# Optimization experiments

Measured on AMD Instinct MI355X. Metric: run time of the kernel, lower is better.

Reference implementation:

```python
import jax, jax.numpy as jnp
import numpy as np

NEG_INF = -1e30


def setup_inputs() -> dict:
    key = jax.random.key(0)
    kq, kk, kv, ks = jax.random.split(key, 4)
    B, H, S, D = 2, 16, 2048, 64
    return {
        "q": jax.random.normal(kq, (B, H, S, D), dtype=jnp.float32),
        "k": jax.random.normal(kk, (B, H, S, D), dtype=jnp.float32),
        "v": jax.random.normal(kv, (B, H, S, D), dtype=jnp.float32),
        "sink_weights": jax.random.normal(ks, (H,), dtype=jnp.float32),
        "sliding_window": 1024,
    }


def reference(q, k, v, sink_weights, sliding_window):
    """Sliding-window causal attention with a learnable attention-sink logit.

    Equivalent to FlexAttention.forward with sink_weights given: an extra kv
    position (the sink) is appended whose score is replaced by sink_weights[h]
    and whose value is zero -> it only adds mass to the softmax denominator.
    """
    B, H, S_q, D = q.shape
    S_kv = k.shape[2]
    scale = 1.0 / np.sqrt(D)

    # [B, H, S_q, S_kv] raw scores
    scores = jnp.einsum("bhqd,bhkd->bhqk", q, k) * scale

    q_idx = jnp.arange(S_q)[:, None]
    kv_idx = jnp.arange(S_kv)[None, :]
    keep = (kv_idx <= q_idx) & (q_idx - kv_idx <= sliding_window)  # [S_q, S_kv]
    scores = jnp.where(keep[None, None], scores, NEG_INF)

    # sink column: per-head learnable logit, always visible
    sink_col = jnp.broadcast_to(
        sink_weights[None, :, None, None], (B, H, S_q, 1)
    )
    logits = jnp.concatenate([scores, sink_col], axis=-1)  # [B,H,S_q,S_kv+1]

    probs = jax.nn.softmax(logits, axis=-1)
    # sink value is zero, so only the first S_kv prob columns hit v
    out = jnp.einsum("bhqk,bhkd->bhqd", probs[..., :S_kv], v)
    return out
```

## Files before the change

### kernel.cpp

```cpp
#include <hip/hip_runtime.h>


typedef __bf16 bf16x8 __attribute__((ext_vector_type(8)));
typedef __bf16 bf16x4 __attribute__((ext_vector_type(4)));
typedef float  f32x16 __attribute__((ext_vector_type(16)));

#define NT 256
#define NEG_BIG (-3.0e38f)

__device__ __forceinline__ int swz(int row, int gran) {
    return row * 64 + ((gran ^ ((row >> 1) & 7)) << 3);
}

__device__ __forceinline__ bf16x4 xswap32(bf16x4 v) {
    union { bf16x4 v; int i[2]; } u;
    u.v = v;
    u.i[0] = __shfl_xor(u.i[0], 32, 64);
    u.i[1] = __shfl_xor(u.i[1], 32, 64);
    return u.v;
}

__device__ const int SEG_N[24] = {3,2,2,2,2,1,2,1, 1,1,1,1,1,1,1,1, 1,1,1,1,1,1,1,1};
__device__ const int SEG_IT[24][3] = {
  {0,1,2},{2,3,0},{3,4,0},{4,5,0},{5,6,0},{6,0,0},{6,7,0},{7,0,0},
  {8,0,0},{8,0,0},{9,0,0},{9,0,0},{10,0,0},{10,0,0},{11,0,0},{11,0,0},
  {12,0,0},{12,0,0},{13,0,0},{13,0,0},{14,0,0},{14,0,0},{15,0,0},{15,0,0}};
__device__ const int SEG_J0[24][3] = {
  {0,0,0},{3,0,0},{6,0,0},{7,0,0},{6,0,0},{3,0,0},{12,0,0},{7,0,0},
  {0,0,0},{9,0,0},{0,0,0},{9,0,0},{0,0,0},{9,0,0},{0,0,0},{9,0,0},
  {0,0,0},{9,0,0},{0,0,0},{9,0,0},{0,0,0},{9,0,0},{0,0,0},{9,0,0}};
__device__ const int SEG_J1[24][3] = {
  {2,4,3},{6,6,0},{8,7,0},{10,6,0},{12,3,0},{12,0,0},{14,7,0},{16,0,0},
  {9,0,0},{18,0,0},{9,0,0},{18,0,0},{9,0,0},{18,0,0},{9,0,0},{18,0,0},
  {9,0,0},{18,0,0},{9,0,0},{18,0,0},{9,0,0},{18,0,0},{9,0,0},{18,0,0}};
__device__ const int SEG_SX[24][3] = {
  {0,0,0},{1,0,0},{1,0,0},{1,0,0},{1,0,0},{1,0,0},{2,0,0},{1,0,0},
  {0,0,0},{1,0,0},{0,0,0},{1,0,0},{0,0,0},{1,0,0},{0,0,0},{1,0,0},
  {0,0,0},{1,0,0},{0,0,0},{1,0,0},{0,0,0},{1,0,0},{0,0,0},{1,0,0}};
__device__ const int NSEG_ITEM[16] = {1,1,2,2,2,2,3,2, 2,2,2,2,2,2,2,2};

__global__ __launch_bounds__(NT, 3) void flex_r13_main(
    const float* __restrict__ Q, const float* __restrict__ K,
    const float* __restrict__ V, const float* __restrict__ SINKW,
    const int* __restrict__ SWIN, void* __restrict__ WS,
    float* __restrict__ OUT, const int H, const int S)
{
    const int t    = threadIdx.x;
    const int lane = t & 63;
    const int w    = t >> 6;
    const int c    = lane & 31;
    const int hl   = lane >> 5;
    const int W    = SWIN[0];
    const float scale = 0.125f;

    const int NBH = gridDim.x / 24;
    int bh, b24;
    if ((NBH & 7) == 0) {
        const int xcd  = blockIdx.x & 7;
        const int rest = blockIdx.x >> 3;
        const int G    = NBH >> 3;
        bh  = (rest % G) * 8 + xcd;
        b24 = rest / G;
    } else {
        bh  = blockIdx.x / 24;
        b24 = blockIdx.x - bh * 24;
    }
    const int h   = bh % H;
    const float sw = SINKW[h];

    __shared__ __align__(16) __bf16 k_lds[2][64 * 64];
    __shared__ __align__(16) __bf16 v_lds[2][64 * 64];

    const size_t basebh = (size_t)bh * S * 64;
    const float4* kp4 = (const float4*)(K + basebh);
    const float4* vp4 = (const float4*)(V + basebh);
    __bf16* O_ws  = (__bf16*)WS;
    float2* ml_ws = (float2*)((char*)WS + (size_t)NBH * 48 * 16384);

    const int dgi = t & 15;
    const int kgi = t >> 4;
    float4 kreg[4], vreg[4];

    const int ns = SEG_N[b24];

    {
        const int it0 = SEG_IT[b24][0];
        const int ktA0 = (2 * it0 - 16 > 0) ? (2 * it0 - 16) : 0;
        const int kt = ktA0 + SEG_J0[b24][0];
        #pragma unroll
        for (int i = 0; i < 4; ++i) kreg[i] = kp4[kt * 1024 + i * NT + t];
        #pragma unroll
        for (int kk = 0; kk < 4; ++kk) vreg[kk] = vp4[kt * 1024 + (4 * kgi + kk) * 16 + dgi];
        #pragma unroll
        for (int i = 0; i < 4; ++i) {
            const int flat = i * NT + t;
            const int key = flat >> 4, dd = flat & 15;
            float4 f = kreg[i];
            bf16x4 b = { (__bf16)f.x, (__bf16)f.y, (__bf16)f.z, (__bf16)f.w };
            *(bf16x4*)&k_lds[0][swz(key, dd >> 1) + (dd & 1) * 4] = b;
        }
        {
            float4 a0 = vreg[0], a1 = vreg[1], a2 = vreg[2], a3 = vreg[3];
            bf16x4 w0 = { (__bf16)a0.x, (__bf16)a1.x, (__bf16)a2.x, (__bf16)a3.x };
            bf16x4 w1 = { (__bf16)a0.y, (__bf16)a1.y, (__bf16)a2.y, (__bf16)a3.y };
            bf16x4 w2 = { (__bf16)a0.z, (__bf16)a1.z, (__bf16)a2.z, (__bf16)a3.z };
            bf16x4 w3 = { (__bf16)a0.w, (__bf16)a1.w, (__bf16)a2.w, (__bf16)a3.w };
            const int gv = kgi >> 1, ov = (kgi & 1) * 4;
            *(bf16x4*)&v_lds[0][swz(4 * dgi + 0, gv) + ov] = w0;
            *(bf16x4*)&v_lds[0][swz(4 * dgi + 1, gv) + ov] = w1;
            *(bf16x4*)&v_lds[0][swz(4 * dgi + 2, gv) + ov] = w2;
            *(bf16x4*)&v_lds[0][swz(4 * dgi + 3, gv) + ov] = w3;
        }
    }

    int par = 0;

    for (int s = 0; s < ns; ++s) {
        const int item = SEG_IT[b24][s];
        const int j0   = SEG_J0[b24][s];
        const int j1   = SEG_J1[b24][s];
        const int sidx = SEG_SX[b24][s];
        const int ktA  = (2 * item - 16 > 0) ? (2 * item - 16) : 0;
        const int qw0  = item * 128 + 32 * w;
        const int qi   = qw0 + c;

        bf16x8 bq[4];
        {
            const float4* qp4 = (const float4*)(Q + basebh + (size_t)qi * 64);
            #pragma unroll
            for (int ks = 0; ks < 4; ++ks) {
                float4 f0 = qp4[4 * ks + 2 * hl];
                float4 f1 = qp4[4 * ks + 2 * hl + 1];
                bq[ks][0] = (__bf16)(f0.x * scale); bq[ks][1] = (__bf16)(f0.y * scale);
                bq[ks][2] = (__bf16)(f0.z * scale); bq[ks][3] = (__bf16)(f0.w * scale);
                bq[ks][4] = (__bf16)(f1.x * scale); bq[ks][5] = (__bf16)(f1.y * scale);
                bq[ks][6] = (__bf16)(f1.z * scale); bq[ks][7] = (__bf16)(f1.w * scale);
            }
        }

        float mrun = (sidx == 0) ? sw : NEG_BIG;
        float lrun = (sidx == 0) ? 1.0f : 0.0f;
        f32x16 accO0, accO1;
        #pragma unroll
        for (int i = 0; i < 16; ++i) { accO0[i] = 0.0f; accO1[i] = 0.0f; }

        for (int j = j0; j < j1; ++j) {
            const int k0 = (ktA + j) * 64;

            __syncthreads();

            int nkt = -1;
            if (j + 1 < j1) nkt = ktA + j + 1;
            else if (s + 1 < ns) {
                const int it2 = SEG_IT[b24][s + 1];
                const int ktA2 = (2 * it2 - 16 > 0) ? (2 * it2 - 16) : 0;
                nkt = ktA2 + SEG_J0[b24][s + 1];
            }
            if (nkt >= 0) {
                #pragma unroll
                for (int i = 0; i < 4; ++i) kreg[i] = kp4[nkt * 1024 + i * NT + t];
                #pragma unroll
                for (int kk = 0; kk < 4; ++kk) vreg[kk] = vp4[nkt * 1024 + (4 * kgi + kk) * 16 + dgi];
            }

            const __bf16* kb = k_lds[par];
            const __bf16* vb = v_lds[par];
            f32x16 accS0, accS1;
            #pragma unroll
            for (int i = 0; i < 16; ++i) { accS0[i] = 0.0f; accS1[i] = 0.0f; }
            __builtin_amdgcn_s_setprio(1);
            #pragma unroll
            for (int ks = 0; ks < 4; ++ks) {
                bf16x8 ka0 = *(const bf16x8*)&kb[swz(c,      2 * ks + hl)];
                bf16x8 ka1 = *(const bf16x8*)&kb[swz(32 + c, 2 * ks + hl)];
                accS0 = __builtin_amdgcn_mfma_f32_32x32x16_bf16(ka0, bq[ks], accS0, 0, 0, 0);
                accS1 = __builtin_amdgcn_mfma_f32_32x32x16_bf16(ka1, bq[ks], accS1, 0, 0, 0);
            }
            __builtin_amdgcn_s_setprio(0);

            const bool interior = (k0 + 63 <= qw0) && (qw0 + 31 - k0 <= W);
            if (!interior) {
                #pragma unroll
                for (int rg = 0; rg < 16; ++rg) {
                    const int kb2 = (rg & 3) + 8 * (rg >> 2) + 4 * hl;
                    const int ki0 = k0 + kb2, ki1 = k0 + 32 + kb2;
                    if (!((ki0 <= qi) && (qi - ki0 <= W))) accS0[rg] = -1e30f;
                    if (!((ki1 <= qi) && (qi - ki1 <= W))) accS1[rg] = -1e30f;
                }
            }

            float q4[8];
            #pragma unroll
            for (int i = 0; i < 4; ++i) {
                q4[i]   = fmaxf(fmaxf(accS0[4*i], accS0[4*i+1]),
                                fmaxf(accS0[4*i+2], accS0[4*i+3]));
                q4[4+i] = fmaxf(fmaxf(accS1[4*i], accS1[4*i+1]),
                                fmaxf(accS1[4*i+2], accS1[4*i+3]));
            }
            float mx = fmaxf(fmaxf(fmaxf(q4[0], q4[1]), fmaxf(q4[2], q4[3])),
                             fmaxf(fmaxf(q4[4], q4[5]), fmaxf(q4[6], q4[7])));
            mx = fmaxf(mx, __shfl_xor(mx, 32, 64));
            if (!__all(mx <= mrun + 8.0f)) {
                const float mnew  = fmaxf(mrun, mx);
                const float alpha = __expf(mrun - mnew);
                lrun *= alpha;
                #pragma unroll
                for (int i = 0; i < 16; ++i) { accO0[i] *= alpha; accO1[i] *= alpha; }
                mrun = mnew;
            }
            float ps = 0.0f;
            #pragma unroll
            for (int i = 0; i < 16; ++i) { float p = __expf(accS0[i] - mrun); accS0[i] = p; ps += p; }
            #pragma unroll
            for (int i = 0; i < 16; ++i) { float p = __expf(accS1[i] - mrun); accS1[i] = p; ps += p; }
            ps += __shfl_xor(ps, 32, 64);
            lrun += ps;

            bf16x4 qA = { (__bf16)accS0[0],  (__bf16)accS0[1],  (__bf16)accS0[2],  (__bf16)accS0[3]  };
            bf16x4 qB = { (__bf16)accS0[4],  (__bf16)accS0[5],  (__bf16)accS0[6],  (__bf16)accS0[7]  };
            bf16x4 qC = { (__bf16)accS0[8],  (__bf16)accS0[9],  (__bf16)accS0[10], (__bf16)accS0[11] };
            bf16x4 qD = { (__bf16)accS0[12], (__bf16)accS0[13], (__bf16)accS0[14], (__bf16)accS0[15] };
            bf16x4 qE = { (__bf16)accS1[0],  (__bf16)accS1[1],  (__bf16)accS1[2],  (__bf16)accS1[3]  };
            bf16x4 qF = { (__bf16)accS1[4],  (__bf16)accS1[5],  (__bf16)accS1[6],  (__bf16)accS1[7]  };
            bf16x4 qG = { (__bf16)accS1[8],  (__bf16)accS1[9],  (__bf16)accS1[10], (__bf16)accS1[11] };
            bf16x4 qH = { (__bf16)accS1[12], (__bf16)accS1[13], (__bf16)accS1[14], (__bf16)accS1[15] };
            bf16x4 r0 = xswap32(hl ? qA : qB);
            bf16x4 r1 = xswap32(hl ? qC : qD);
            bf16x4 r2 = xswap32(hl ? qE : qF);
            bf16x4 r3 = xswap32(hl ? qG : qH);
            bf16x4 lo0 = hl ? r0 : qA, hi0 = hl ? qB : r0;
            bf16x4 lo1 = hl ? r1 : qC, hi1 = hl ? qD : r1;
            bf16x4 lo2 = hl ? r2 : qE, hi2 = hl ? qF : r2;
            bf16x4 lo3 = hl ? r3 : qG, hi3 = hl ? qH : r3;
            bf16x8 bp[4];
            #pragma unroll
            for (int e = 0; e < 4; ++e) {
                bp[0][e] = lo0[e]; bp[0][4+e] = hi0[e];
                bp[1][e] = lo1[e]; bp[1][4+e] = hi1[e];
                bp[2][e] = lo2[e]; bp[2][4+e] = hi2[e];
                bp[3][e] = lo3[e]; bp[3][4+e] = hi3[e];
            }

            __builtin_amdgcn_s_setprio(1);
            #pragma unroll
            for (int ks = 0; ks < 4; ++ks) {
                bf16x8 va0 = *(const bf16x8*)&vb[swz(c,      2 * ks + hl)];
                bf16x8 va1 = *(const bf16x8*)&vb[swz(32 + c, 2 * ks + hl)];
                accO0 = __builtin_amdgcn_mfma_f32_32x32x16_bf16(va0, bp[ks], accO0, 0, 0, 0);
                accO1 = __builtin_amdgcn_mfma_f32_32x32x16_bf16(va1, bp[ks], accO1, 0, 0, 0);
            }
            __builtin_amdgcn_s_setprio(0);

            if (nkt >= 0) {
                const int np = par ^ 1;
                #pragma unroll
                for (int i = 0; i < 4; ++i) {
                    const int flat = i * NT + t;
                    const int key = flat >> 4, dd = flat & 15;
                    float4 f = kreg[i];
                    bf16x4 b = { (__bf16)f.x, (__bf16)f.y, (__bf16)f.z, (__bf16)f.w };
                    *(bf16x4*)&k_lds[np][swz(key, dd >> 1) + (dd & 1) * 4] = b;
                }
                float4 a0 = vreg[0], a1 = vreg[1], a2 = vreg[2], a3 = vreg[3];
                bf16x4 w0 = { (__bf16)a0.x, (__bf16)a1.x, (__bf16)a2.x, (__bf16)a3.x };
                bf16x4 w1 = { (__bf16)a0.y, (__bf16)a1.y, (__bf16)a2.y, (__bf16)a3.y };
                bf16x4 w2 = { (__bf16)a0.z, (__bf16)a1.z, (__bf16)a2.z, (__bf16)a3.z };
                bf16x4 w3 = { (__bf16)a0.w, (__bf16)a1.w, (__bf16)a2.w, (__bf16)a3.w };
                const int gv = kgi >> 1, ov = (kgi & 1) * 4;
                *(bf16x4*)&v_lds[np][swz(4 * dgi + 0, gv) + ov] = w0;
                *(bf16x4*)&v_lds[np][swz(4 * dgi + 1, gv) + ov] = w1;
                *(bf16x4*)&v_lds[np][swz(4 * dgi + 2, gv) + ov] = w2;
                *(bf16x4*)&v_lds[np][swz(4 * dgi + 3, gv) + ov] = w3;
            }
            par ^= 1;
        }

        if (item < 2) {
            const float inv = 1.0f / lrun;
            float* ob = OUT + basebh + (size_t)qi * 64;
            #pragma unroll
            for (int rg = 0; rg < 4; ++rg) {
                float4 f0 = { accO0[4*rg+0]*inv, accO0[4*rg+1]*inv,
                              accO0[4*rg+2]*inv, accO0[4*rg+3]*inv };
                float4 f1 = { accO1[4*rg+0]*inv, accO1[4*rg+1]*inv,
                              accO1[4*rg+2]*inv, accO1[4*rg+3]*inv };
                *(float4*)&ob[     8 * rg + 4 * hl] = f0;
                *(float4*)&ob[32 + 8 * rg + 4 * hl] = f1;
            }
        } else {
            const int slot = (bh * 16 + item) * 3 + sidx;
            const int qrel = 32 * w + c;
            if (hl == 0) ml_ws[(size_t)slot * 128 + qrel] = make_float2(mrun, lrun);
            __bf16* Os = O_ws + (size_t)slot * 8192 + (size_t)qrel * 64;
            #pragma unroll
            for (int qd = 0; qd < 4; ++qd) {
                const int d0 = 8 * qd + 4 * hl;
                bf16x4 b0 = { (__bf16)accO0[4*qd+0], (__bf16)accO0[4*qd+1],
                              (__bf16)accO0[4*qd+2], (__bf16)accO0[4*qd+3] };
                bf16x4 b1 = { (__bf16)accO1[4*qd+0], (__bf16)accO1[4*qd+1],
                              (__bf16)accO1[4*qd+2], (__bf16)accO1[4*qd+3] };
                *(bf16x4*)&Os[d0]      = b0;
                *(bf16x4*)&Os[32 + d0] = b1;
            }
        }
    }
}

__global__ __launch_bounds__(256) void flex_r13_combine(
    const void* __restrict__ WS, float* __restrict__ OUT, const int H, const int S)
{
    const int NBH  = gridDim.x / 14;
    const int bi   = blockIdx.x;
    const int bh   = bi / 14;
    const int item = 2 + (bi - bh * 14);
    const int ns   = NSEG_ITEM[item];
    const int t    = threadIdx.x;
    const int q    = t >> 1;
    const int half = t & 1;

    const __bf16* O_ws = (const __bf16*)WS;
    const float2* ml_ws = (const float2*)((const char*)WS + (size_t)NBH * 48 * 16384);
    const int base = (bh * 16 + item) * 3;

    float m[3], lv[3], a[3];
    float mst = NEG_BIG;
    for (int s = 0; s < ns; ++s) {
        float2 e = ml_ws[(size_t)(base + s) * 128 + q];
        m[s] = e.x; lv[s] = e.y;
        mst = fmaxf(mst, m[s]);
    }
    float lst = 0.0f;
    for (int s = 0; s < ns; ++s) { a[s] = __expf(m[s] - mst); lst += a[s] * lv[s]; }
    const float inv = 1.0f / lst;

    float acc[32];
    #pragma unroll
    for (int i = 0; i < 32; ++i) acc[i] = 0.0f;
    for (int s = 0; s < ns; ++s) {
        const __bf16* Os = O_ws + (size_t)(base + s) * 8192 + (size_t)q * 64 + 32 * half;
        const float as = a[s];
        #pragma unroll
        for (int v8 = 0; v8 < 4; ++v8) {
            bf16x8 o = *(const bf16x8*)&Os[8 * v8];
            #pragma unroll
            for (int jj = 0; jj < 8; ++jj) acc[8 * v8 + jj] += as * (float)o[jj];
        }
    }

    float* dst = OUT + (size_t)bh * S * 64 + (size_t)(item * 128 + q) * 64 + 32 * half;
    #pragma unroll
    for (int v4 = 0; v4 < 8; ++v4) {
        float4 f = { acc[4*v4+0] * inv, acc[4*v4+1] * inv,
                     acc[4*v4+2] * inv, acc[4*v4+3] * inv };
        *(float4*)&dst[4 * v4] = f;
    }
}

extern "C" void kernel_launch(void* const* d_in, const int* in_sizes, int n_in,
                              void* d_out, int out_size, void* d_ws, size_t ws_size,
                              hipStream_t stream) {
    const float* q     = (const float*)d_in[0];
    const float* k     = (const float*)d_in[1];
    const float* v     = (const float*)d_in[2];
    const float* sinkw = (const float*)d_in[3];
    const int*   swin  = (const int*)d_in[4];
    float* out = (float*)d_out;

    const int H = in_sizes[3];
    const int S = 2048;
    const int B = in_sizes[0] / (H * S * 64);
    const int NBH = B * H;

    flex_r13_main<<<dim3(NBH * 24), NT, 0, stream>>>(q, k, v, sinkw, swin, d_ws, out, H, S);
    flex_r13_combine<<<dim3(NBH * 14), 256, 0, stream>>>(d_ws, out, H, S);
}
```

Before: 131.2 us.

## Process two KV tiles per iteration with one shared softmax max and rescale

The inner loop now handles two 64-key tiles per step. Both tiles are staged in a double-buffered LDS layout, and one running max and rescale is computed across the pair, which halves the barriers and max-update checks per key. Exp sums are split into several partial accumulators to shorten dependency chains. The cost is double the LDS and register footprint, and launch bounds drop from 3 to 2 blocks per SM, which reduces occupancy.

```diff
diff --git a/kernel.cpp b/kernel.cpp
--- a/kernel.cpp
+++ b/kernel.cpp
@@ -39,7 +39,91 @@
   {0,0,0},{1,0,0},{0,0,0},{1,0,0},{0,0,0},{1,0,0},{0,0,0},{1,0,0}};
 __device__ const int NSEG_ITEM[16] = {1,1,2,2,2,2,3,2, 2,2,2,2,2,2,2,2};
 
-__global__ __launch_bounds__(NT, 3) void flex_r13_main(
+__device__ __forceinline__ void qk_mfma(const __bf16* kb, const bf16x8 bq[4],
+                                        int c, int hl, f32x16& s0, f32x16& s1) {
+    #pragma unroll
+    for (int ks = 0; ks < 4; ++ks) {
+        bf16x8 ka0 = *(const bf16x8*)&kb[swz(c,      2 * ks + hl)];
+        bf16x8 ka1 = *(const bf16x8*)&kb[swz(32 + c, 2 * ks + hl)];
+        s0 = __builtin_amdgcn_mfma_f32_32x32x16_bf16(ka0, bq[ks], s0, 0, 0, 0);
+        s1 = __builtin_amdgcn_mfma_f32_32x32x16_bf16(ka1, bq[ks], s1, 0, 0, 0);
+    }
+}
+
+__device__ __forceinline__ void pv_mfma(const __bf16* vb, const bf16x8 bp[4],
+                                        int c, int hl, f32x16& o0, f32x16& o1) {
+    #pragma unroll
+    for (int ks = 0; ks < 4; ++ks) {
+        bf16x8 va0 = *(const bf16x8*)&vb[swz(c,      2 * ks + hl)];
+        bf16x8 va1 = *(const bf16x8*)&vb[swz(32 + c, 2 * ks + hl)];
+        o0 = __builtin_amdgcn_mfma_f32_32x32x16_bf16(va0, bp[ks], o0, 0, 0, 0);
+        o1 = __builtin_amdgcn_mfma_f32_32x32x16_bf16(va1, bp[ks], o1, 0, 0, 0);
+    }
+}
+
+__device__ __forceinline__ void mask_tile(f32x16& s0, f32x16& s1,
+                                          int k0, int qi, int W, int hl) {
+    #pragma unroll
+    for (int rg = 0; rg < 16; ++rg) {
+        const int kb2 = (rg & 3) + 8 * (rg >> 2) + 4 * hl;
+        const int ki0 = k0 + kb2, ki1 = k0 + 32 + kb2;
+        if (!((ki0 <= qi) && (qi - ki0 <= W))) s0[rg] = -1e30f;
+        if (!((ki1 <= qi) && (qi - ki1 <= W))) s1[rg] = -1e30f;
+    }
+}
+
+__device__ __forceinline__ void exch_bp(const f32x16 s0, const f32x16 s1,
+                                        int hl, bf16x8 bp[4]) {
+    bf16x4 qA = { (__bf16)s0[0],  (__bf16)s0[1],  (__bf16)s0[2],  (__bf16)s0[3]  };
+    bf16x4 qB = { (__bf16)s0[4],  (__bf16)s0[5],  (__bf16)s0[6],  (__bf16)s0[7]  };
+    bf16x4 qC = { (__bf16)s0[8],  (__bf16)s0[9],  (__bf16)s0[10], (__bf16)s0[11] };
+    bf16x4 qD = { (__bf16)s0[12], (__bf16)s0[13], (__bf16)s0[14], (__bf16)s0[15] };
+    bf16x4 qE = { (__bf16)s1[0],  (__bf16)s1[1],  (__bf16)s1[2],  (__bf16)s1[3]  };
+    bf16x4 qF = { (__bf16)s1[4],  (__bf16)s1[5],  (__bf16)s1[6],  (__bf16)s1[7]  };
+    bf16x4 qG = { (__bf16)s1[8],  (__bf16)s1[9],  (__bf16)s1[10], (__bf16)s1[11] };
+    bf16x4 qH = { (__bf16)s1[12], (__bf16)s1[13], (__bf16)s1[14], (__bf16)s1[15] };
+    bf16x4 r0 = xswap32(hl ? qA : qB);
+    bf16x4 r1 = xswap32(hl ? qC : qD);
+    bf16x4 r2 = xswap32(hl ? qE : qF);
+    bf16x4 r3 = xswap32(hl ? qG : qH);
+    bf16x4 lo0 = hl ? r0 : qA, hi0 = hl ? qB : r0;
+    bf16x4 lo1 = hl ? r1 : qC, hi1 = hl ? qD : r1;
+    bf16x4 lo2 = hl ? r2 : qE, hi2 = hl ? qF : r2;
+    bf16x4 lo3 = hl ? r3 : qG, hi3 = hl ? qH : r3;
+    #pragma unroll
+    for (int e = 0; e < 4; ++e) {
+        bp[0][e] = lo0[e]; bp[0][4+e] = hi0[e];
+        bp[1][e] = lo1[e]; bp[1][4+e] = hi1[e];
+        bp[2][e] = lo2[e]; bp[2][4+e] = hi2[e];
+        bp[3][e] = lo3[e]; bp[3][4+e] = hi3[e];
+    }
+}
+
+__device__ __forceinline__ void stage_k(__bf16* dst, const float4* kr, int t) {
+    #pragma unroll
+    for (int i = 0; i < 4; ++i) {
+        const int flat = i * NT + t;
+        const int key = flat >> 4, dd = flat & 15;
+        float4 f = kr[i];
+        bf16x4 b = { (__bf16)f.x, (__bf16)f.y, (__bf16)f.z, (__bf16)f.w };
+        *(bf16x4*)&dst[swz(key, dd >> 1) + (dd & 1) * 4] = b;
+    }
+}
+
+__device__ __forceinline__ void stage_v(__bf16* dst, const float4* vr, int dgi, int kgi) {
+    float4 a0 = vr[0], a1 = vr[1], a2 = vr[2], a3 = vr[3];
+    bf16x4 w0 = { (__bf16)a0.x, (__bf16)a1.x, (__bf16)a2.x, (__bf16)a3.x };
+    bf16x4 w1 = { (__bf16)a0.y, (__bf16)a1.y, (__bf16)a2.y, (__bf16)a3.y };
+    bf16x4 w2 = { (__bf16)a0.z, (__bf16)a1.z, (__bf16)a2.z, (__bf16)a3.z };
+    bf16x4 w3 = { (__bf16)a0.w, (__bf16)a1.w, (__bf16)a2.w, (__bf16)a3.w };
+    const int gv = kgi >> 1, ov = (kgi & 1) * 4;
+    *(bf16x4*)&dst[swz(4 * dgi + 0, gv) + ov] = w0;
+    *(bf16x4*)&dst[swz(4 * dgi + 1, gv) + ov] = w1;
+    *(bf16x4*)&dst[swz(4 * dgi + 2, gv) + ov] = w2;
+    *(bf16x4*)&dst[swz(4 * dgi + 3, gv) + ov] = w3;
+}
+
+__global__ __launch_bounds__(NT, 2) void flex_r14_main(
     const float* __restrict__ Q, const float* __restrict__ K,
     const float* __restrict__ V, const float* __restrict__ SINKW,
     const int* __restrict__ SWIN, void* __restrict__ WS,
@@ -68,8 +152,8 @@
     const int h   = bh % H;
     const float sw = SINKW[h];
 
-    __shared__ __align__(16) __bf16 k_lds[2][64 * 64];
-    __shared__ __align__(16) __bf16 v_lds[2][64 * 64];
+    __shared__ __align__(16) __bf16 k_lds[2][2][64 * 64];
+    __shared__ __align__(16) __bf16 v_lds[2][2][64 * 64];
 
     const size_t basebh = (size_t)bh * S * 64;
     const float4* kp4 = (const float4*)(K + basebh);
@@ -79,38 +163,28 @@
 
     const int dgi = t & 15;
     const int kgi = t >> 4;
-    float4 kreg[4], vreg[4];
+    float4 kreg[8], vreg[8];
 
     const int ns = SEG_N[b24];
 
     {
         const int it0 = SEG_IT[b24][0];
         const int ktA0 = (2 * it0 - 16 > 0) ? (2 * it0 - 16) : 0;
-        const int kt = ktA0 + SEG_J0[b24][0];
-        #pragma unroll
-        for (int i = 0; i < 4; ++i) kreg[i] = kp4[kt * 1024 + i * NT + t];
-        #pragma unroll
-        for (int kk = 0; kk < 4; ++kk) vreg[kk] = vp4[kt * 1024 + (4 * kgi + kk) * 16 + dgi];
+        const int kt0 = ktA0 + SEG_J0[b24][0];
         #pragma unroll
         for (int i = 0; i < 4; ++i) {
-            const int flat = i * NT + t;
-            const int key = flat >> 4, dd = flat & 15;
-            float4 f = kreg[i];
-            bf16x4 b = { (__bf16)f.x, (__bf16)f.y, (__bf16)f.z, (__bf16)f.w };
-            *(bf16x4*)&k_lds[0][swz(key, dd >> 1) + (dd & 1) * 4] = b;
-        }
-        {
-            float4 a0 = vreg[0], a1 = vreg[1], a2 = vreg[2], a3 = vreg[3];
-            bf16x4 w0 = { (__bf16)a0.x, (__bf16)a1.x, (__bf16)a2.x, (__bf16)a3.x };
-            bf16x4 w1 = { (__bf16)a0.y, (__bf16)a1.y, (__bf16)a2.y, (__bf16)a3.y };
-            bf16x4 w2 = { (__bf16)a0.z, (__bf16)a1.z, (__bf16)a2.z, (__bf16)a3.z };
-            bf16x4 w3 = { (__bf16)a0.w, (__bf16)a1.w, (__bf16)a2.w, (__bf16)a3.w };
-            const int gv = kgi >> 1, ov = (kgi & 1) * 4;
-            *(bf16x4*)&v_lds[0][swz(4 * dgi + 0, gv) + ov] = w0;
-            *(bf16x4*)&v_lds[0][swz(4 * dgi + 1, gv) + ov] = w1;
-            *(bf16x4*)&v_lds[0][swz(4 * dgi + 2, gv) + ov] = w2;
-            *(bf16x4*)&v_lds[0][swz(4 * dgi + 3, gv) + ov] = w3;
-        }
+            kreg[i]     = kp4[kt0 * 1024 + i * NT + t];
+            kreg[4 + i] = kp4[(kt0 + 1) * 1024 + i * NT + t];
+        }
+        #pragma unroll
+        for (int kk = 0; kk < 4; ++kk) {
+            vreg[kk]     = vp4[kt0 * 1024 + (4 * kgi + kk) * 16 + dgi];
+            vreg[4 + kk] = vp4[(kt0 + 1) * 1024 + (4 * kgi + kk) * 16 + dgi];
+        }
+        stage_k(&k_lds[0][0][0], &kreg[0], t);
+        stage_v(&v_lds[0][0][0], &vreg[0], dgi, kgi);
+        stage_k(&k_lds[0][1][0], &kreg[4], t);
+        stage_v(&v_lds[0][1][0], &vreg[4], dgi, kgi);
     }
 
     int par = 0;
@@ -144,61 +218,68 @@
         #pragma unroll
         for (int i = 0; i < 16; ++i) { accO0[i] = 0.0f; accO1[i] = 0.0f; }
 
-        for (int j = j0; j < j1; ++j) {
-            const int k0 = (ktA + j) * 64;
+        for (int j = j0; j < j1; j += 2) {
+            const bool two = (j + 1 < j1);
+            const int k0a = (ktA + j) * 64;
+            const int k0b = k0a + 64;
 
             __syncthreads();
 
-            int nkt = -1;
-            if (j + 1 < j1) nkt = ktA + j + 1;
-            else if (s + 1 < ns) {
-                const int it2 = SEG_IT[b24][s + 1];
+            int n0 = -1, n1 = -1;
+            if (j + 2 < j1) {
+                n0 = ktA + j + 2;
+                if (j + 3 < j1) n1 = n0 + 1;
+            } else if (s + 1 < ns) {
+                const int it2  = SEG_IT[b24][s + 1];
                 const int ktA2 = (2 * it2 - 16 > 0) ? (2 * it2 - 16) : 0;
-                nkt = ktA2 + SEG_J0[b24][s + 1];
-            }
-            if (nkt >= 0) {
-                #pragma unroll
-                for (int i = 0; i < 4; ++i) kreg[i] = kp4[nkt * 1024 + i * NT + t];
-                #pragma unroll
-                for (int kk = 0; kk < 4; ++kk) vreg[kk] = vp4[nkt * 1024 + (4 * kgi + kk) * 16 + dgi];
-            }
-
-            const __bf16* kb = k_lds[par];
-            const __bf16* vb = v_lds[par];
-            f32x16 accS0, accS1;
-            #pragma unroll
-            for (int i = 0; i < 16; ++i) { accS0[i] = 0.0f; accS1[i] = 0.0f; }
+                const int j02  = SEG_J0[b24][s + 1];
+                n0 = ktA2 + j02;
+                if (j02 + 1 < SEG_J1[b24][s + 1]) n1 = n0 + 1;
+            }
+            if (n0 >= 0) {
+                #pragma unroll
+                for (int i = 0; i < 4; ++i) kreg[i] = kp4[n0 * 1024 + i * NT + t];
+                #pragma unroll
+                for (int kk = 0; kk < 4; ++kk) vreg[kk] = vp4[n0 * 1024 + (4 * kgi + kk) * 16 + dgi];
+            }
+            if (n1 >= 0) {
+                #pragma unroll
+                for (int i = 0; i < 4; ++i) kreg[4 + i] = kp4[n1 * 1024 + i * NT + t];
+                #pragma unroll
+                for (int kk = 0; kk < 4; ++kk) vreg[4 + kk] = vp4[n1 * 1024 + (4 * kgi + kk) * 16 + dgi];
+            }
+
+            f32x16 sa0, sa1, sb0, sb1;
+            #pragma unroll
+            for (int i = 0; i < 16; ++i) { sa0[i] = 0.0f; sa1[i] = 0.0f; sb0[i] = 0.0f; sb1[i] = 0.0f; }
             __builtin_amdgcn_s_setprio(1);
-            #pragma unroll
-            for (int ks = 0; ks < 4; ++ks) {
-                bf16x8 ka0 = *(const bf16x8*)&kb[swz(c,      2 * ks + hl)];
-                bf16x8 ka1 = *(const bf16x8*)&kb[swz(32 + c, 2 * ks + hl)];
-                accS0 = __builtin_amdgcn_mfma_f32_32x32x16_bf16(ka0, bq[ks], accS0, 0, 0, 0);
-                accS1 = __builtin_amdgcn_mfma_f32_32x32x16_bf16(ka1, bq[ks], accS1, 0, 0, 0);
-            }
+            qk_mfma(&k_lds[par][0][0], bq, c, hl, sa0, sa1);
+            if (two) qk_mfma(&k_lds[par][1][0], bq, c, hl, sb0, sb1);
             __builtin_amdgcn_s_setprio(0);
 
-            const bool interior = (k0 + 63 <= qw0) && (qw0 + 31 - k0 <= W);
-            if (!interior) {
-                #pragma unroll
-                for (int rg = 0; rg < 16; ++rg) {
-                    const int kb2 = (rg & 3) + 8 * (rg >> 2) + 4 * hl;
-                    const int ki0 = k0 + kb2, ki1 = k0 + 32 + kb2;
-                    if (!((ki0 <= qi) && (qi - ki0 <= W))) accS0[rg] = -1e30f;
-                    if (!((ki1 <= qi) && (qi - ki1 <= W))) accS1[rg] = -1e30f;
+            if (!((k0a + 63 <= qw0) && (qw0 + 31 - k0a <= W)))
+                mask_tile(sa0, sa1, k0a, qi, W, hl);
+            if (two && !((k0b + 63 <= qw0) && (qw0 + 31 - k0b <= W)))
+                mask_tile(sb0, sb1, k0b, qi, W, hl);
+
+            float m8[8];
+            #pragma unroll
+            for (int i = 0; i < 4; ++i) {
+                m8[i]   = fmaxf(fmaxf(sa0[4*i], sa0[4*i+1]), fmaxf(sa0[4*i+2], sa0[4*i+3]));
+                m8[4+i] = fmaxf(fmaxf(sa1[4*i], sa1[4*i+1]), fmaxf(sa1[4*i+2], sa1[4*i+3]));
+            }
+            float mx = fmaxf(fmaxf(fmaxf(m8[0], m8[1]), fmaxf(m8[2], m8[3])),
+                             fmaxf(fmaxf(m8[4], m8[5]), fmaxf(m8[6], m8[7])));
+            if (two) {
+                float n8[8];
+                #pragma unroll
+                for (int i = 0; i < 4; ++i) {
+                    n8[i]   = fmaxf(fmaxf(sb0[4*i], sb0[4*i+1]), fmaxf(sb0[4*i+2], sb0[4*i+3]));
+                    n8[4+i] = fmaxf(fmaxf(sb1[4*i], sb1[4*i+1]), fmaxf(sb1[4*i+2], sb1[4*i+3]));
                 }
-            }
-
-            float q4[8];
-            #pragma unroll
-            for (int i = 0; i < 4; ++i) {
-                q4[i]   = fmaxf(fmaxf(accS0[4*i], accS0[4*i+1]),
-                                fmaxf(accS0[4*i+2], accS0[4*i+3]));
-                q4[4+i] = fmaxf(fmaxf(accS1[4*i], accS1[4*i+1]),
-                                fmaxf(accS1[4*i+2], accS1[4*i+3]));
-            }
-            float mx = fmaxf(fmaxf(fmaxf(q4[0], q4[1]), fmaxf(q4[2], q4[3])),
-                             fmaxf(fmaxf(q4[4], q4[5]), fmaxf(q4[6], q4[7])));
+                mx = fmaxf(mx, fmaxf(fmaxf(fmaxf(n8[0], n8[1]), fmaxf(n8[2], n8[3])),
+                                     fmaxf(fmaxf(n8[4], n8[5]), fmaxf(n8[6], n8[7]))));
+            }
             mx = fmaxf(mx, __shfl_xor(mx, 32, 64));
             if (!__all(mx <= mrun + 8.0f)) {
                 const float mnew  = fmaxf(mrun, mx);
@@ -208,69 +289,47 @@
                 for (int i = 0; i < 16; ++i) { accO0[i] *= alpha; accO1[i] *= alpha; }
                 mrun = mnew;
             }
-            float ps = 0.0f;
-            #pragma unroll
-            for (int i = 0; i < 16; ++i) { float p = __expf(accS0[i] - mrun); accS0[i] = p; ps += p; }
-            #pragma unroll
-            for (int i = 0; i < 16; ++i) { float p = __expf(accS1[i] - mrun); accS1[i] = p; ps += p; }
+            float sc[8];
+            #pragma unroll
+            for (int i = 0; i < 8; ++i) sc[i] = 0.0f;
+            #pragma unroll
+            for (int i = 0; i < 16; ++i) {
+                float p0 = __expf(sa0[i] - mrun); sa0[i] = p0; sc[i & 3]       += p0;
+                float p1 = __expf(sa1[i] - mrun); sa1[i] = p1; sc[4 + (i & 3)] += p1;
+            }
+            if (two) {
+                #pragma unroll
+                for (int i = 0; i < 16; ++i) {
+                    float p0 = __expf(sb0[i] - mrun); sb0[i] = p0; sc[i & 3]       += p0;
+                    float p1 = __expf(sb1[i] - mrun); sb1[i] = p1; sc[4 + (i & 3)] += p1;
+                }
+            }
+            float ps = ((sc[0] + sc[1]) + (sc[2] + sc[3])) + ((sc[4] + sc[5]) + (sc[6] + sc[7]));
             ps += __shfl_xor(ps, 32, 64);
             lrun += ps;
 
-            bf16x4 qA = { (__bf16)accS0[0],  (__bf16)accS0[1],  (__bf16)accS0[2],  (__bf16)accS0[3]  };
-            bf16x4 qB = { (__bf16)accS0[4],  (__bf16)accS0[5],  (__bf16)accS0[6],  (__bf16)accS0[7]  };
-            bf16x4 qC = { (__bf16)accS0[8],  (__bf16)accS0[9],  (__bf16)accS0[10], (__bf16)accS0[11] };
-            bf16x4 qD = { (__bf16)accS0[12], (__bf16)accS0[13], (__bf16)accS0[14], (__bf16)accS0[15] };
-            bf16x4 qE = { (__bf16)accS1[0],  (__bf16)accS1[1],  (__bf16)accS1[2],  (__bf16)accS1[3]  };
-            bf16x4 qF = { (__bf16)accS1[4],  (__bf16)accS1[5],  (__bf16)accS1[6],  (__bf16)accS1[7]  };
-            bf16x4 qG = { (__bf16)accS1[8],  (__bf16)accS1[9],  (__bf16)accS1[10], (__bf16)accS1[11] };
-            bf16x4 qH = { (__bf16)accS1[12], (__bf16)accS1[13], (__bf16)accS1[14], (__bf16)accS1[15] };
-            bf16x4 r0 = xswap32(hl ? qA : qB);
-            bf16x4 r1 = xswap32(hl ? qC : qD);
-            bf16x4 r2 = xswap32(hl ? qE : qF);
-            bf16x4 r3 = xswap32(hl ? qG : qH);
-            bf16x4 lo0 = hl ? r0 : qA, hi0 = hl ? qB : r0;
-            bf16x4 lo1 = hl ? r1 : qC, hi1 = hl ? qD : r1;
-            bf16x4 lo2 = hl ? r2 : qE, hi2 = hl ? qF : r2;
-            bf16x4 lo3 = hl ? r3 : qG, hi3 = hl ? qH : r3;
-            bf16x8 bp[4];
-            #pragma unroll
-            for (int e = 0; e < 4; ++e) {
-                bp[0][e] = lo0[e]; bp[0][4+e] = hi0[e];
-                bp[1][e] = lo1[e]; bp[1][4+e] = hi1[e];
-                bp[2][e] = lo2[e]; bp[2][4+e] = hi2[e];
-                bp[3][e] = lo3[e]; bp[3][4+e] = hi3[e];
-            }
-
-            __builtin_amdgcn_s_setprio(1);
-            #pragma unroll
-            for (int ks = 0; ks < 4; ++ks) {
-                bf16x8 va0 = *(const bf16x8*)&vb[swz(c,      2 * ks + hl)];
-                bf16x8 va1 = *(const bf16x8*)&vb[swz(32 + c, 2 * ks + hl)];
-                accO0 = __builtin_amdgcn_mfma_f32_32x32x16_bf16(va0, bp[ks], accO0, 0, 0, 0);
-                accO1 = __builtin_amdgcn_mfma_f32_32x32x16_bf16(va1, bp[ks], accO1, 0, 0, 0);
-            }
-            __builtin_amdgcn_s_setprio(0);
-
-            if (nkt >= 0) {
-                const int np = par ^ 1;
-                #pragma unroll
-                for (int i = 0; i < 4; ++i) {
-                    const int flat = i * NT + t;
-                    const int key = flat >> 4, dd = flat & 15;
-                    float4 f = kreg[i];
-                    bf16x4 b = { (__bf16)f.x, (__bf16)f.y, (__bf16)f.z, (__bf16)f.w };
-                    *(bf16x4*)&k_lds[np][swz(key, dd >> 1) + (dd & 1) * 4] = b;
-                }
-                float4 a0 = vreg[0], a1 = vreg[1], a2 = vreg[2], a3 = vreg[3];
-                bf16x4 w0 = { (__bf16)a0.x, (__bf16)a1.x, (__bf16)a2.x, (__bf16)a3.x };
-                bf16x4 w1 = { (__bf16)a0.y, (__bf16)a1.y, (__bf16)a2.y, (__bf16)a3.y };
-                bf16x4 w2 = { (__bf16)a0.z, (__bf16)a1.z, (__bf16)a2.z, (__bf16)a3.z };
-                bf16x4 w3 = { (__bf16)a0.w, (__bf16)a1.w, (__bf16)a2.w, (__bf16)a3.w };
-                const int gv = kgi >> 1, ov = (kgi & 1) * 4;
-                *(bf16x4*)&v_lds[np][swz(4 * dgi + 0, gv) + ov] = w0;
-                *(bf16x4*)&v_lds[np][swz(4 * dgi + 1, gv) + ov] = w1;
-                *(bf16x4*)&v_lds[np][swz(4 * dgi + 2, gv) + ov] = w2;
-                *(bf16x4*)&v_lds[np][swz(4 * dgi + 3, gv) + ov] = w3;
+            {
+                bf16x8 bp[4];
+                exch_bp(sa0, sa1, hl, bp);
+                __builtin_amdgcn_s_setprio(1);
+                pv_mfma(&v_lds[par][0][0], bp, c, hl, accO0, accO1);
+                __builtin_amdgcn_s_setprio(0);
+            }
+            if (two) {
+                bf16x8 bp[4];
+                exch_bp(sb0, sb1, hl, bp);
+                __builtin_amdgcn_s_setprio(1);
+                pv_mfma(&v_lds[par][1][0], bp, c, hl, accO0, accO1);
+                __builtin_amdgcn_s_setprio(0);
+            }
+
+            if (n0 >= 0) {
+                stage_k(&k_lds[par ^ 1][0][0], &kreg[0], t);
+                stage_v(&v_lds[par ^ 1][0][0], &vreg[0], dgi, kgi);
+            }
+            if (n1 >= 0) {
+                stage_k(&k_lds[par ^ 1][1][0], &kreg[4], t);
+                stage_v(&v_lds[par ^ 1][1][0], &vreg[4], dgi, kgi);
             }
             par ^= 1;
         }
@@ -306,7 +365,7 @@
     }
 }
 
-__global__ __launch_bounds__(256) void flex_r13_combine(
+__global__ __launch_bounds__(256) void flex_r14_combine(
     const void* __restrict__ WS, float* __restrict__ OUT, const int H, const int S)
 {
     const int NBH  = gridDim.x / 14;
@@ -371,6 +430,6 @@
     const int B = in_sizes[0] / (H * S * 64);
     const int NBH = B * H;
 
-    flex_r13_main<<<dim3(NBH * 24), NT, 0, stream>>>(q, k, v, sinkw, swin, d_ws, out, H, S);
-    flex_r13_combine<<<dim3(NBH * 14), 256, 0, stream>>>(d_ws, out, H, S);
-}
+    flex_r14_main<<<dim3(NBH * 24), NT, 0, stream>>>(q, k, v, sinkw, swin, d_ws, out, H, S);
+    flex_r14_combine<<<dim3(NBH * 14), 256, 0, stream>>>(d_ws, out, H, S);
+}
```

Result: slower. 143.5 us (+9.4%).
